# Optimization experiments

Hardware: AMD Instinct MI355X
Metric: run time of the kernel (lower is better)

The kernel has to match this reference:

```python
import jax, jax.numpy as jnp
import numpy as np

H = 16  # attention heads


def setup_inputs() -> dict:
    key = jax.random.key(0)
    k0, k1, k2 = jax.random.split(key, 3)
    B, T, C = 2, 2048, 1024
    x = jax.random.normal(k0, (B, T, C), dtype=jnp.float32)
    W_attn = jax.random.normal(k1, (3 * C, C), dtype=jnp.float32) * 0.02
    W_proj = jax.random.normal(k2, (C, C), dtype=jnp.float32) * 0.02
    b_proj = jnp.zeros((C,), dtype=jnp.float32)
    return {"x": x, "W_attn": W_attn, "W_proj": W_proj, "b_proj": b_proj}


def reference(x, W_attn, W_proj, b_proj):
    # Eval-mode (dropout = identity), rotational_embeddings=False, flash=False path.
    B, T, C = x.shape
    d = C // H
    qkv = jnp.einsum('btc,fc->btf', x, W_attn)          # [B,T,3C] fused QKV proj
    q, k, v = jnp.split(qkv, 3, axis=-1)
    # [B,T,C] -> [B,H,T,d]
    q = q.reshape(B, T, H, d).transpose(0, 2, 1, 3)
    k = k.reshape(B, T, H, d).transpose(0, 2, 1, 3)
    v = v.reshape(B, T, H, d).transpose(0, 2, 1, 3)
    scale = 1.0 / np.sqrt(d).astype(np.float32)
    att = jnp.einsum('bhqd,bhkd->bhqk', q, k) * scale    # full TxT scores (no mask)
    att = jax.nn.softmax(att, axis=-1)
    y = jnp.einsum('bhqk,bhkd->bhqd', att, v)            # [B,H,T,d]
    y = y.transpose(0, 2, 1, 3).reshape(B, T, C)
    return jnp.einsum('btc,oc->bto', y, W_proj) + b_proj
```

## Files before the change

kernel.cpp:

```cpp
#include <hip/hip_runtime.h>
#include <hip/hip_bf16.h>
#include <stdint.h>

typedef __attribute__((ext_vector_type(8))) short bf16x8;
typedef __attribute__((ext_vector_type(4))) float f32x4;
typedef __attribute__((ext_vector_type(4))) unsigned u32x4;

#define MFMA16(A,B,C) __builtin_amdgcn_mfma_f32_16x16x32_bf16(A,B,C,0,0,0)


__device__ inline void gld_lds16(const __hip_bfloat16* g, __hip_bfloat16* l) {
  __builtin_amdgcn_global_load_lds(
      (const __attribute__((address_space(1))) void*)g,
      (__attribute__((address_space(3))) void*)l, 16, 0, 0);
}

__device__ inline unsigned pkbf(float a, float b) {
  __hip_bfloat162 t = __float22bfloat162_rn(float2{a, b});
  return *(unsigned*)&t;
}

__device__ inline void quad_mix(unsigned &a, unsigned &b) {
#if __has_builtin(__builtin_amdgcn_permlane32_swap) && __has_builtin(__builtin_amdgcn_permlane16_swap)
  auto r1 = __builtin_amdgcn_permlane32_swap(a, b, false, false);
  auto r2 = __builtin_amdgcn_permlane16_swap(r1[0], r1[1], false, false);
  a = r2[0];
  b = r2[1];
#else
  int lane = (int)(threadIdx.x & 63);
  int g = lane >> 4;
  int lm = lane & 15;
  int slo = (((g << 1) & 3) << 4) | lm;
  int shi = ((((g << 1) | 1) & 3) << 4) | lm;
  unsigned t0 = (unsigned)__shfl((int)a, slo, 64);
  unsigned t1 = (unsigned)__shfl((int)b, slo, 64);
  unsigned t2 = (unsigned)__shfl((int)a, shi, 64);
  unsigned t3 = (unsigned)__shfl((int)b, shi, 64);
  bool hi = g >= 2;
  unsigned na = hi ? t1 : t0;
  unsigned nb = hi ? t3 : t2;
  a = na;
  b = nb;
#endif
}

__global__ __launch_bounds__(256)
void cvt_bf16(const float* __restrict__ s0, __hip_bfloat16* __restrict__ d0, int n0,
              const float* __restrict__ s1, __hip_bfloat16* __restrict__ d1, int n1,
              const float* __restrict__ s2, __hip_bfloat16* __restrict__ d2, int n2)
{
  const float* s; __hip_bfloat16* d; int n;
  if      (blockIdx.y == 0) { s = s0; d = d0; n = n0; }
  else if (blockIdx.y == 1) { s = s1; d = d1; n = n1; }
  else                      { s = s2; d = d2; n = n2; }
  int idx = (blockIdx.x * 256 + threadIdx.x) * 8;
  if (idx >= n) return;
  float4 u0 = *(const float4*)(s + idx);
  float4 u1 = *(const float4*)(s + idx + 4);
  __hip_bfloat16 t[8];
  t[0] = __float2bfloat16(u0.x); t[1] = __float2bfloat16(u0.y);
  t[2] = __float2bfloat16(u0.z); t[3] = __float2bfloat16(u0.w);
  t[4] = __float2bfloat16(u1.x); t[5] = __float2bfloat16(u1.y);
  t[6] = __float2bfloat16(u1.z); t[7] = __float2bfloat16(u1.w);
  *(int4*)(d + idx) = *(const int4*)t;
}

template<int BM, int BN, typename TC>
__global__ __launch_bounds__(256)
void gemm_bt(const __hip_bfloat16* __restrict__ A,
             const __hip_bfloat16* __restrict__ B,
             TC* __restrict__ C,
             const float* __restrict__ bias,
             __hip_bfloat16* __restrict__ vtg,
             int M, int N, int K)
{
  constexpr int MI = BM / 32;
  constexpr int NJ = BN / 32;
  constexpr int NP = (BM + BN) / 64;

  __shared__ __align__(16) __hip_bfloat16 As[BM * 32];
  __shared__ __align__(16) __hip_bfloat16 Bs[BN * 32];

  const int tid  = threadIdx.x;
  const int lane = tid & 63;
  const int w    = tid >> 6;
  const int lm   = lane & 15;
  const int g    = lane >> 4;

  const int bm = blockIdx.y * BM;
  const int bn = blockIdx.x * BN;
  const int rm = (w >> 1) * (BM / 2);
  const int cn = (w & 1) * (BN / 2);

  const f32x4 fzero = {0.0f, 0.0f, 0.0f, 0.0f};
  f32x4 acc[MI][NJ];
  for (int i = 0; i < MI; i++)
    for (int j = 0; j < NJ; j++)
      acc[i][j] = fzero;

  for (int k0 = 0; k0 < K; k0 += 32) {
    __syncthreads();
#pragma unroll
    for (int p = 0; p < NP; p++) {
      int c = tid + p * 256;
      if (c < BM * 4)
        gld_lds16(&A[(size_t)(bm + (c >> 2)) * K + k0 + (c & 3) * 8], &As[c * 8]);
      else {
        int cb = c - BM * 4;
        gld_lds16(&B[(size_t)(bn + (cb >> 2)) * K + k0 + (cb & 3) * 8], &Bs[cb * 8]);
      }
    }
    __syncthreads();

    bf16x8 af[MI], bfr[NJ];
#pragma unroll
    for (int i = 0; i < MI; i++)
      af[i] = *(const bf16x8*)&As[(rm + 16 * i + lm) * 32 + 8 * g];
#pragma unroll
    for (int j = 0; j < NJ; j++)
      bfr[j] = *(const bf16x8*)&Bs[(cn + 16 * j + lm) * 32 + 8 * g];
#pragma unroll
    for (int i = 0; i < MI; i++)
#pragma unroll
      for (int j = 0; j < NJ; j++)
        acc[i][j] = MFMA16(af[i], bfr[j], acc[i][j]);
  }

  if (vtg != nullptr && bn >= 2048) {
#pragma unroll
    for (int j = 0; j < NJ; j++) {
      int colv = bn + cn + 16 * j + lm - 2048;
      int vh = colv >> 6, dd = colv & 63;
#pragma unroll
      for (int i = 0; i < MI; i++) {
        int m0 = bm + rm + 16 * i + 4 * g;
        int bb = m0 >> 11, t0 = m0 & 2047;
        __hip_bfloat16 t4[4];
#pragma unroll
        for (int r = 0; r < 4; r++) t4[r] = __float2bfloat16(acc[i][j][r]);
        *(int2*)&vtg[((size_t)(bb * 16 + vh) * 64 + dd) * 2048 + t0] =
            *(const int2*)t4;
      }
    }
    return;
  }

  const float qs = (vtg != nullptr && bn < 1024) ? (0.125f * 1.4426950408889634f)
                                                 : 1.0f;
#pragma unroll
  for (int j = 0; j < NJ; j++) {
    int coln = bn + cn + 16 * j + lm;
    float bv = bias ? bias[coln] : 0.0f;
#pragma unroll
    for (int i = 0; i < MI; i++) {
#pragma unroll
      for (int r = 0; r < 4; r++) {
        int rowm = bm + rm + 16 * i + 4 * g + r;
        float v = acc[i][j][r] * qs + bv;
        if constexpr (sizeof(TC) == 2)
          C[(size_t)rowm * N + coln] = __float2bfloat16(v);
        else
          C[(size_t)rowm * N + coln] = v;
      }
    }
  }
}

__global__ __launch_bounds__(256)
void mha(const __hip_bfloat16* __restrict__ qkv,
         const __hip_bfloat16* __restrict__ vtg,
         __hip_bfloat16* __restrict__ yout,
         __hip_bfloat16* __restrict__ po,
         float* __restrict__ pl,
         int nsteps)
{
  const int T = 2048, F = 3072, Cc = 1024;
  const int bh = blockIdx.y;
  const int b  = bh >> 4, h = bh & 15;
  const int qb0 = blockIdx.x * 128;
  const int z   = blockIdx.z;
  const int kvb = z * 64 * nsteps;

  const int tid  = threadIdx.x;
  const int lane = tid & 63;
  const int w    = tid >> 6;
  const int lm   = lane & 15;
  const int g    = lane >> 4;

  __shared__ __align__(16) __hip_bfloat16 Ks[2][64 * 64];
  __shared__ __align__(16) __hip_bfloat16 Vs[2][64 * 64];

  const size_t rowbase = (size_t)b * T * F;
  const int hoff = h * 64;
  const __hip_bfloat16* Kbase = qkv + rowbase + 1024 + hoff;
  const __hip_bfloat16* Vtb   = vtg + (size_t)(b * 16 + h) * 64 * 2048;

  const int qw = qb0 + 32 * w;
  bf16x8 aq[2][2];
#pragma unroll
  for (int mt = 0; mt < 2; mt++)
#pragma unroll
    for (int e = 0; e < 2; e++)
      aq[mt][e] = *(const bf16x8*)
          &qkv[rowbase + (size_t)(qw + 16 * mt + lm) * F + hoff + 32 * e + 8 * g];

  const f32x4 fzero = {0.0f, 0.0f, 0.0f, 0.0f};
  const short one_bf = (short)0x3f80;
  const bf16x8 vone = {one_bf, one_bf, one_bf, one_bf,
                       one_bf, one_bf, one_bf, one_bf};
  f32x4 yacc[2][4];
  f32x4 yl[2];
#pragma unroll
  for (int mt = 0; mt < 2; mt++) {
    yl[mt] = fzero;
#pragma unroll
    for (int c = 0; c < 4; c++) yacc[mt][c] = fzero;
  }

  const int sx = lm & 7;

  auto stage = [&](int tt, int bb) {
    const int kvn = kvb + tt * 64;
#pragma unroll
    for (int p = 0; p < 2; p++) {
      int c = tid + p * 256;
      int row = c >> 3, sl = c & 7, gc = sl ^ (row & 7);
      gld_lds16(Kbase + (size_t)(kvn + row) * F + gc * 8, &Ks[bb][c * 8]);
    }
#pragma unroll
    for (int p = 0; p < 2; p++) {
      int c = tid + p * 256;
      int row = c >> 3, sl = c & 7, gc = sl ^ (row & 7);
      gld_lds16(Vtb + (size_t)row * 2048 + kvn + gc * 8, &Vs[bb][c * 8]);
    }
  };

  stage(0, 0);

  for (int t = 0; t < nsteps; t++) {
    const int buf = t & 1;
    __syncthreads();
    if (t + 1 < nsteps) stage(t + 1, buf ^ 1);

    const __hip_bfloat16* Kb = Ks[buf];
    const __hip_bfloat16* Vb = Vs[buf];

    f32x4 st[2][4];
    __builtin_amdgcn_s_setprio(1);
#pragma unroll
    for (int c2 = 0; c2 < 4; c2++) {
      bf16x8 k0 = *(const bf16x8*)&Kb[(16 * c2 + lm) * 64 + ((0 + g) ^ sx) * 8];
      bf16x8 k1 = *(const bf16x8*)&Kb[(16 * c2 + lm) * 64 + ((4 + g) ^ sx) * 8];
      st[0][c2] = MFMA16(k0, aq[0][0], fzero);
      st[0][c2] = MFMA16(k1, aq[0][1], st[0][c2]);
      st[1][c2] = MFMA16(k0, aq[1][0], fzero);
      st[1][c2] = MFMA16(k1, aq[1][1], st[1][c2]);
    }
    __builtin_amdgcn_s_setprio(0);

    bf16x8 ap[2][2];
#pragma unroll
    for (int mt = 0; mt < 2; mt++) {
#pragma unroll
      for (int hf = 0; hf < 2; hf++) {
        unsigned pkv[2][2];
#pragma unroll
        for (int cc = 0; cc < 2; cc++) {
          const f32x4 &s4 = st[mt][2 * hf + cc];
#pragma unroll
          for (int u = 0; u < 2; u++) {
            float p0 = __builtin_amdgcn_exp2f(s4[2 * u]);
            float p1 = __builtin_amdgcn_exp2f(s4[2 * u + 1]);
            pkv[cc][u] = pkbf(p0, p1);
          }
        }
        unsigned f0 = pkv[0][0], f2 = pkv[1][0];
        quad_mix(f0, f2);
        unsigned f1 = pkv[0][1], f3 = pkv[1][1];
        quad_mix(f1, f3);
        u32x4 fv = {f0, f1, f2, f3};
        ap[mt][hf] = __builtin_bit_cast(bf16x8, fv);
      }
    }

    __builtin_amdgcn_s_setprio(1);
#pragma unroll
    for (int c = 0; c < 4; c++) {
#pragma unroll
      for (int hf = 0; hf < 2; hf++) {
        bf16x8 bv = *(const bf16x8*)
            &Vb[(16 * c + lm) * 64 + (((hf << 2) | g) ^ sx) * 8];
        yacc[0][c] = MFMA16(ap[0][hf], bv, yacc[0][c]);
        yacc[1][c] = MFMA16(ap[1][hf], bv, yacc[1][c]);
      }
    }
#pragma unroll
    for (int mt = 0; mt < 2; mt++) {
      yl[mt] = MFMA16(ap[mt][0], vone, yl[mt]);
      yl[mt] = MFMA16(ap[mt][1], vone, yl[mt]);
    }
    __builtin_amdgcn_s_setprio(0);
  }

#pragma unroll
  for (int mt = 0; mt < 2; mt++) {
    if (yout != nullptr) {
      float rv[4];
#pragma unroll
      for (int r = 0; r < 4; r++)
        rv[r] = 1.0f / yl[mt][r];
#pragma unroll
      for (int c = 0; c < 4; c++)
#pragma unroll
        for (int r = 0; r < 4; r++) {
          int qrow = qw + 16 * mt + 4 * g + r;
          yout[(size_t)(b * T + qrow) * Cc + hoff + 16 * c + lm] =
              __float2bfloat16(yacc[mt][c][r] * rv[r]);
        }
    } else {
      __hip_bfloat16* pz = po + (size_t)z * 4096 * 1024;
      float* plz = pl + (size_t)z * 4096 * 16;
#pragma unroll
      for (int c = 0; c < 4; c++)
#pragma unroll
        for (int r = 0; r < 4; r++) {
          int qrow = qw + 16 * mt + 4 * g + r;
          pz[(size_t)(b * T + qrow) * Cc + hoff + 16 * c + lm] =
              __float2bfloat16(yacc[mt][c][r]);
        }
      if (lm == 0) {
#pragma unroll
        for (int r = 0; r < 4; r++)
          plz[(b * T + qw + 16 * mt + 4 * g + r) * 16 + h] = yl[mt][r];
      }
    }
  }
}

template<int Z>
__global__ __launch_bounds__(256)
void combine(const __hip_bfloat16* __restrict__ po,
             const float* __restrict__ pl,
             __hip_bfloat16* __restrict__ y)
{
  int idx = (blockIdx.x * 256 + threadIdx.x) * 8;
  int row = idx >> 10, c = idx & 1023, h = c >> 6;
  float l = 0.0f;
#pragma unroll
  for (int zi = 0; zi < Z; zi++)
    l += pl[zi * 4096 * 16 + row * 16 + h];
  float rinv = 1.0f / l;
  float acc[8] = {0.f, 0.f, 0.f, 0.f, 0.f, 0.f, 0.f, 0.f};
#pragma unroll
  for (int zi = 0; zi < Z; zi++) {
    int4 raw = *(const int4*)(po + (size_t)zi * 4096 * 1024 + idx);
    const __hip_bfloat16* pa = (const __hip_bfloat16*)&raw;
#pragma unroll
    for (int j = 0; j < 8; j++) acc[j] += __bfloat162float(pa[j]);
  }
  __hip_bfloat16 t[8];
#pragma unroll
  for (int j = 0; j < 8; j++) t[j] = __float2bfloat16(acc[j] * rinv);
  *(int4*)(y + idx) = *(const int4*)t;
}

extern "C" void kernel_launch(void* const* d_in, const int* in_sizes, int n_in,
                              void* d_out, int out_size, void* d_ws, size_t ws_size,
                              hipStream_t stream)
{
  const float* x  = (const float*)d_in[0];
  const float* Wa = (const float*)d_in[1];
  const float* Wp = (const float*)d_in[2];
  const float* bp = (const float*)d_in[3];
  float* out = (float*)d_out;

  const int BT = 4096, C = 1024, F3 = 3072;
  char* ws = (char*)d_ws;
  __hip_bfloat16* qkv  = (__hip_bfloat16*)ws;
  __hip_bfloat16* vtg  = (__hip_bfloat16*)(ws + 25165824);
  __hip_bfloat16* xbf  = (__hip_bfloat16*)(ws + 33554432);
  __hip_bfloat16* yb   = xbf;
  __hip_bfloat16* Wabf = (__hip_bfloat16*)(ws + 41943040);
  __hip_bfloat16* Wpbf = (__hip_bfloat16*)(ws + 48234496);
  __hip_bfloat16* Opar = (__hip_bfloat16*)(ws + 50331648);
  float*          lpar = (float*)(ws + 67108864);
  const size_t need_split = 67633152;

  cvt_bf16<<<dim3(2048, 3), 256, 0, stream>>>(
      x, xbf, BT * C, Wa, Wabf, F3 * C, Wp, Wpbf, C * C);
  gemm_bt<128, 128, __hip_bfloat16>
      <<<dim3(F3 / 128, BT / 128), 256, 0, stream>>>(xbf, Wabf, qkv, nullptr, vtg,
                                                     BT, F3, C);
  if (ws_size >= need_split) {
    mha<<<dim3(16, 32, 2), 256, 0, stream>>>(qkv, vtg, nullptr, Opar, lpar, 16);
    combine<2><<<dim3(BT * C / 2048), 256, 0, stream>>>(Opar, lpar, yb);
  } else {
    mha<<<dim3(16, 32, 1), 256, 0, stream>>>(qkv, vtg, yb, nullptr, nullptr, 32);
  }
  gemm_bt<64, 128, float>
      <<<dim3(C / 128, BT / 64), 256, 0, stream>>>(yb, Wpbf, out, bp, nullptr,
                                                   BT, C, C);
}
```

Baseline: 207.7 us.

## Fuse split-KV combine into output projection GEMM and coalesce V-transpose stores

The separate combine kernel is removed. The output-projection GEMM now loads both partial attention outputs, sums them, and normalises by the summed softmax denominators while staging A into LDS. The QKV GEMM's transposed-V epilogue goes through an LDS scratch tile, so each lane writes 16-byte rows instead of scattered 8-byte stores. The MHA grid is reordered so heads vary fastest. This saves one launch and a full round trip of y through memory. In exchange the fused A-tile loads become synchronous register loads instead of async global-to-LDS copies, and the divide is recomputed for every K tile.

```diff
diff --git a/kernel.cpp b/kernel.cpp
--- a/kernel.cpp
+++ b/kernel.cpp
@@ -65,21 +65,25 @@
   *(int4*)(d + idx) = *(const int4*)t;
 }
 
-template<int BM, int BN, typename TC>
+template<int BM, int BN, typename TC, bool VT, bool FUSE>
 __global__ __launch_bounds__(256)
 void gemm_bt(const __hip_bfloat16* __restrict__ A,
              const __hip_bfloat16* __restrict__ B,
              TC* __restrict__ C,
              const float* __restrict__ bias,
              __hip_bfloat16* __restrict__ vtg,
+             const float* __restrict__ pl,
              int M, int N, int K)
 {
   constexpr int MI = BM / 32;
   constexpr int NJ = BN / 32;
   constexpr int NP = (BM + BN) / 64;
-
-  __shared__ __align__(16) __hip_bfloat16 As[BM * 32];
-  __shared__ __align__(16) __hip_bfloat16 Bs[BN * 32];
+  constexpr int SMEM_E = VT ? (((BM + BN) * 32 > 4 * 64 * 72) ? (BM + BN) * 32
+                                                              : 4 * 64 * 72)
+                            : (BM + BN) * 32;
+  __shared__ __align__(16) __hip_bfloat16 smem[SMEM_E];
+  __hip_bfloat16* As = smem;
+  __hip_bfloat16* Bs = smem + BM * 32;
 
   const int tid  = threadIdx.x;
   const int lane = tid & 63;
@@ -103,9 +107,28 @@
 #pragma unroll
     for (int p = 0; p < NP; p++) {
       int c = tid + p * 256;
-      if (c < BM * 4)
-        gld_lds16(&A[(size_t)(bm + (c >> 2)) * K + k0 + (c & 3) * 8], &As[c * 8]);
-      else {
+      if (c < BM * 4) {
+        if constexpr (FUSE) {
+          int row = bm + (c >> 2);
+          int col = k0 + (c & 3) * 8;
+          int hh  = col >> 6;
+          float li = pl[row * 16 + hh] + pl[(size_t)M * 16 + row * 16 + hh];
+          float rinv = 1.0f / li;
+          int4 ra = *(const int4*)&A[(size_t)row * K + col];
+          int4 rb = *(const int4*)&A[(size_t)M * K + (size_t)row * K + col];
+          const __hip_bfloat16* pa = (const __hip_bfloat16*)&ra;
+          const __hip_bfloat16* pb = (const __hip_bfloat16*)&rb;
+          __hip_bfloat16 tt[8];
+#pragma unroll
+          for (int jj = 0; jj < 8; jj++)
+            tt[jj] = __float2bfloat16(
+                (__bfloat162float(pa[jj]) + __bfloat162float(pb[jj])) * rinv);
+          *(int4*)&As[c * 8] = *(const int4*)tt;
+        } else {
+          gld_lds16(&A[(size_t)(bm + (c >> 2)) * K + k0 + (c & 3) * 8],
+                    &As[c * 8]);
+        }
+      } else {
         int cb = c - BM * 4;
         gld_lds16(&B[(size_t)(bn + (cb >> 2)) * K + k0 + (cb & 3) * 8], &Bs[cb * 8]);
       }
@@ -126,27 +149,39 @@
         acc[i][j] = MFMA16(af[i], bfr[j], acc[i][j]);
   }
 
-  if (vtg != nullptr && bn >= 2048) {
-#pragma unroll
-    for (int j = 0; j < NJ; j++) {
-      int colv = bn + cn + 16 * j + lm - 2048;
-      int vh = colv >> 6, dd = colv & 63;
-#pragma unroll
-      for (int i = 0; i < MI; i++) {
-        int m0 = bm + rm + 16 * i + 4 * g;
-        int bb = m0 >> 11, t0 = m0 & 2047;
-        __hip_bfloat16 t4[4];
-#pragma unroll
-        for (int r = 0; r < 4; r++) t4[r] = __float2bfloat16(acc[i][j][r]);
-        *(int2*)&vtg[((size_t)(bb * 16 + vh) * 64 + dd) * 2048 + t0] =
-            *(const int2*)t4;
-      }
-    }
-    return;
-  }
-
-  const float qs = (vtg != nullptr && bn < 1024) ? (0.125f * 1.4426950408889634f)
-                                                 : 1.0f;
+  if constexpr (VT) {
+    if (vtg != nullptr && bn >= 2048) {
+      __syncthreads();
+      __hip_bfloat16* scr = smem + w * (64 * 72);
+      const int h  = (bn + cn - 2048) >> 6;
+      const int bb = bm >> 11;
+      const int t0 = (bm & 2047) + rm;
+#pragma unroll
+      for (int j = 0; j < NJ; j++) {
+        int dd = 16 * j + lm;
+#pragma unroll
+        for (int i = 0; i < MI; i++) {
+          __hip_bfloat16 t4[4];
+#pragma unroll
+          for (int r = 0; r < 4; r++) t4[r] = __float2bfloat16(acc[i][j][r]);
+          *(int2*)&scr[dd * 72 + 16 * i + 4 * g] = *(const int2*)t4;
+        }
+      }
+      asm volatile("s_waitcnt lgkmcnt(0)" ::: "memory");
+      const int u = lane & 7, ddl = lane >> 3;
+#pragma unroll
+      for (int it = 0; it < 8; it++) {
+        int dd = it * 8 + ddl;
+        int4 vrow = *(const int4*)&scr[dd * 72 + u * 8];
+        *(int4*)&vtg[((size_t)(bb * 16 + h) * 64 + dd) * 2048 + t0 + u * 8] =
+            vrow;
+      }
+      return;
+    }
+  }
+
+  const float qs = (VT && vtg != nullptr && bn < 1024)
+                       ? (0.125f * 1.4426950408889634f) : 1.0f;
 #pragma unroll
   for (int j = 0; j < NJ; j++) {
     int coln = bn + cn + 16 * j + lm;
@@ -175,9 +210,9 @@
          int nsteps)
 {
   const int T = 2048, F = 3072, Cc = 1024;
-  const int bh = blockIdx.y;
+  const int bh = blockIdx.x;
   const int b  = bh >> 4, h = bh & 15;
-  const int qb0 = blockIdx.x * 128;
+  const int qb0 = blockIdx.y * 128;
   const int z   = blockIdx.z;
   const int kvb = z * 64 * nsteps;
 
@@ -337,33 +372,6 @@
   }
 }
 
-template<int Z>
-__global__ __launch_bounds__(256)
-void combine(const __hip_bfloat16* __restrict__ po,
-             const float* __restrict__ pl,
-             __hip_bfloat16* __restrict__ y)
-{
-  int idx = (blockIdx.x * 256 + threadIdx.x) * 8;
-  int row = idx >> 10, c = idx & 1023, h = c >> 6;
-  float l = 0.0f;
-#pragma unroll
-  for (int zi = 0; zi < Z; zi++)
-    l += pl[zi * 4096 * 16 + row * 16 + h];
-  float rinv = 1.0f / l;
-  float acc[8] = {0.f, 0.f, 0.f, 0.f, 0.f, 0.f, 0.f, 0.f};
-#pragma unroll
-  for (int zi = 0; zi < Z; zi++) {
-    int4 raw = *(const int4*)(po + (size_t)zi * 4096 * 1024 + idx);
-    const __hip_bfloat16* pa = (const __hip_bfloat16*)&raw;
-#pragma unroll
-    for (int j = 0; j < 8; j++) acc[j] += __bfloat162float(pa[j]);
-  }
-  __hip_bfloat16 t[8];
-#pragma unroll
-  for (int j = 0; j < 8; j++) t[j] = __float2bfloat16(acc[j] * rinv);
-  *(int4*)(y + idx) = *(const int4*)t;
-}
-
 extern "C" void kernel_launch(void* const* d_in, const int* in_sizes, int n_in,
                               void* d_out, int out_size, void* d_ws, size_t ws_size,
                               hipStream_t stream)
@@ -388,16 +396,18 @@
 
   cvt_bf16<<<dim3(2048, 3), 256, 0, stream>>>(
       x, xbf, BT * C, Wa, Wabf, F3 * C, Wp, Wpbf, C * C);
-  gemm_bt<128, 128, __hip_bfloat16>
+  gemm_bt<128, 128, __hip_bfloat16, true, false>
       <<<dim3(F3 / 128, BT / 128), 256, 0, stream>>>(xbf, Wabf, qkv, nullptr, vtg,
-                                                     BT, F3, C);
+                                                     nullptr, BT, F3, C);
   if (ws_size >= need_split) {
-    mha<<<dim3(16, 32, 2), 256, 0, stream>>>(qkv, vtg, nullptr, Opar, lpar, 16);
-    combine<2><<<dim3(BT * C / 2048), 256, 0, stream>>>(Opar, lpar, yb);
+    mha<<<dim3(32, 16, 2), 256, 0, stream>>>(qkv, vtg, nullptr, Opar, lpar, 16);
+    gemm_bt<64, 128, float, false, true>
+        <<<dim3(C / 128, BT / 64), 256, 0, stream>>>(Opar, Wpbf, out, bp,
+                                                     nullptr, lpar, BT, C, C);
   } else {
-    mha<<<dim3(16, 32, 1), 256, 0, stream>>>(qkv, vtg, yb, nullptr, nullptr, 32);
-  }
-  gemm_bt<64, 128, float>
-      <<<dim3(C / 128, BT / 64), 256, 0, stream>>>(yb, Wpbf, out, bp, nullptr,
-                                                   BT, C, C);
-}
+    mha<<<dim3(32, 16, 1), 256, 0, stream>>>(qkv, vtg, yb, nullptr, nullptr, 32);
+    gemm_bt<64, 128, float, false, false>
+        <<<dim3(C / 128, BT / 64), 256, 0, stream>>>(yb, Wpbf, out, bp,
+                                                     nullptr, nullptr, BT, C, C);
+  }
+}
```

Result: slower. 214.5 us (+3.2%).
